# Performance work log

Measured on AMD Instinct MI355X. Metric: run time of the kernel, lower is better.

Reference implementation:

```python
import jax, jax.numpy as jnp
import numpy as np

B, N, D, E, H = 4, 512, 16, 16, 128  # envs, max_node, node_dim, edge_dim, hidden_dim


def setup_inputs() -> dict:
    key = jax.random.key(0)
    ks = jax.random.split(key, 8)
    node_feature = jax.random.normal(ks[0], (B, N, D), dtype=jnp.float32)
    adjacency = (jax.random.uniform(ks[1], (B, N, N)) < 0.05).astype(jnp.float32)
    edge_feature = jax.random.normal(ks[2], (B, N, N, E), dtype=jnp.float32)
    node_mask = jnp.ones((B, N), dtype=jnp.float32)  # unused by the model, kept for signature parity
    # edge_fc: Dense(2*D + E -> H) with relu; feature_fc: Dense(H + D -> H) with relu
    W_edge = jax.random.normal(ks[3], (2 * D + E, H), dtype=jnp.float32) * np.sqrt(2.0 / (2 * D + E)).astype(np.float32)
    b_edge = jnp.zeros((H,), dtype=jnp.float32)
    W_feat = jax.random.normal(ks[4], (H + D, H), dtype=jnp.float32) * np.sqrt(2.0 / (H + D)).astype(np.float32)
    b_feat = jnp.zeros((H,), dtype=jnp.float32)
    return {
        "node_feature": node_feature,
        "adjacency": adjacency,
        "edge_feature": edge_feature,
        "node_mask": node_mask,
        "W_edge": W_edge,
        "b_edge": b_edge,
        "W_feat": W_feat,
        "b_feat": b_feat,
    }


def reference(node_feature, adjacency, edge_feature, node_mask, W_edge, b_edge, W_feat, b_feat):
    d = node_feature.shape[-1]
    # Split edge_fc weight by the concat layout [node_i, node_j, edge]:
    # concat([node_i, node_j, edge]) @ W == node_i@Wi + node_j@Wj + edge@We
    Wi, Wj, We = W_edge[:d], W_edge[d:2 * d], W_edge[2 * d:]
    proj_i = jnp.einsum("bnd,dh->bnh", node_feature, Wi)  # sender (row) projection
    proj_j = jnp.einsum("bnd,dh->bnh", node_feature, Wj)  # receiver (col) projection
    proj_e = jnp.einsum("bije,eh->bijh", edge_feature, We)
    edge_out = jax.nn.relu(proj_i[:, :, None, :] + proj_j[:, None, :, :] + proj_e + b_edge)  # (B,N,N,H)
    # adjacency-masked sum over neighbors j (axis=2)
    message = jnp.einsum("bijh,bij->bih", edge_out, adjacency)  # (B,N,H)
    ending = jax.nn.relu(jnp.concatenate([message, node_feature], axis=-1) @ W_feat + b_feat)  # (B,N,H)
    return ending, edge_out
```

## Files before the change

kernel.cpp:

```cpp
#include <hip/hip_runtime.h>

#define BB 4
#define NN 512
#define DD 16
#define EE 16
#define HH 128

typedef float f32x4 __attribute__((ext_vector_type(4)));

#define LD4(p) (*(const float4*)(p))

__global__ void proj_j_kernel(const float* __restrict__ nf,
                              const float* __restrict__ W_edge,
                              float* __restrict__ pj) {
    int idx = blockIdx.x * 256 + threadIdx.x;
    if (idx >= BB * NN * HH) return;
    int h  = idx & (HH - 1);
    int bj = idx >> 7;
    const float* row = nf + bj * DD;
    float acc = 0.f;
#pragma unroll
    for (int d = 0; d < DD; ++d)
        acc = fmaf(row[d], W_edge[(DD + d) * HH + h], acc);
    pj[idx] = acc;
}

template <bool USE_WS>
__global__ __launch_bounds__(128, 4)
void fused_kernel(const float* __restrict__ node_feature,
                  const float* __restrict__ adjacency,
                  const float* __restrict__ edge_feature,
                  const float* __restrict__ W_edge,
                  const float* __restrict__ b_edge,
                  const float* __restrict__ W_feat,
                  const float* __restrict__ b_feat,
                  const float* __restrict__ pj,
                  float* __restrict__ out_end,
                  float* __restrict__ out_edge) {
    const int bi = blockIdx.x;
    const int b  = bi >> 9;
    const int t  = threadIdx.x;
    const int hq = t & 31;
    const int jl = t >> 5;
    const int h0 = hq * 4;

    float4 we[EE];
#pragma unroll
    for (int e = 0; e < EE; ++e)
        we[e] = LD4(W_edge + (2 * DD + e) * HH + h0);

    float4 wj[USE_WS ? 1 : EE];
    if constexpr (!USE_WS) {
#pragma unroll
        for (int e = 0; e < EE; ++e)
            wj[e] = LD4(W_edge + (DD + e) * HH + h0);
    }

    float4 pi = LD4(b_edge + h0);
    {
        const float* nfi = node_feature + bi * DD;
#pragma unroll
        for (int d4 = 0; d4 < DD; d4 += 4) {
            float4 v = LD4(nfi + d4);
            float nd[4] = {v.x, v.y, v.z, v.w};
#pragma unroll
            for (int q = 0; q < 4; ++q) {
                float4 wi = LD4(W_edge + (d4 + q) * HH + h0);
                pi.x = fmaf(nd[q], wi.x, pi.x);
                pi.y = fmaf(nd[q], wi.y, pi.y);
                pi.z = fmaf(nd[q], wi.z, pi.z);
                pi.w = fmaf(nd[q], wi.w, pi.w);
            }
        }
    }

    const float* efb  = edge_feature + (size_t)bi * NN * EE;
    const float* adjr = adjacency + (size_t)bi * NN;
    const float* pjb  = pj + (b * NN) * HH;
    const float* nfb  = node_feature + (b * NN) * DD;
    float*       eob  = out_edge + (size_t)bi * NN * HH;

    float4 msg = make_float4(0.f, 0.f, 0.f, 0.f);

    int j = jl;
    float4 efA0 = LD4(efb + j * EE + 0);
    float4 efA1 = LD4(efb + j * EE + 4);
    float4 efA2 = LD4(efb + j * EE + 8);
    float4 efA3 = LD4(efb + j * EE + 12);
    float4 pjA  = make_float4(0.f, 0.f, 0.f, 0.f);
    if constexpr (USE_WS) pjA = LD4(pjb + j * HH + h0);
    float  adjA = adjr[j];

    for (int it = 0; it < NN / 4; ++it) {
        const int jn = j + 4;
        const int jc = (jn < NN) ? jn : j;

        float4 efB0 = LD4(efb + jc * EE + 0);
        float4 efB1 = LD4(efb + jc * EE + 4);
        float4 efB2 = LD4(efb + jc * EE + 8);
        float4 efB3 = LD4(efb + jc * EE + 12);
        float4 pjB  = make_float4(0.f, 0.f, 0.f, 0.f);
        if constexpr (USE_WS) pjB = LD4(pjb + jc * HH + h0);
        float  adjB = adjr[jc];

        float4 acc;
        if constexpr (USE_WS) {
            acc.x = pi.x + pjA.x;
            acc.y = pi.y + pjA.y;
            acc.z = pi.z + pjA.z;
            acc.w = pi.w + pjA.w;
        } else {
            acc = pi;
            const float* nfj = nfb + j * DD;
#pragma unroll
            for (int d = 0; d < DD; ++d) {
                float nv = nfj[d];
                acc.x = fmaf(nv, wj[d].x, acc.x);
                acc.y = fmaf(nv, wj[d].y, acc.y);
                acc.z = fmaf(nv, wj[d].z, acc.z);
                acc.w = fmaf(nv, wj[d].w, acc.w);
            }
        }

        float ef_[EE] = {efA0.x, efA0.y, efA0.z, efA0.w,
                         efA1.x, efA1.y, efA1.z, efA1.w,
                         efA2.x, efA2.y, efA2.z, efA2.w,
                         efA3.x, efA3.y, efA3.z, efA3.w};
#pragma unroll
        for (int e = 0; e < EE; ++e) {
            acc.x = fmaf(ef_[e], we[e].x, acc.x);
            acc.y = fmaf(ef_[e], we[e].y, acc.y);
            acc.z = fmaf(ef_[e], we[e].z, acc.z);
            acc.w = fmaf(ef_[e], we[e].w, acc.w);
        }
        acc.x = fmaxf(acc.x, 0.f);
        acc.y = fmaxf(acc.y, 0.f);
        acc.z = fmaxf(acc.z, 0.f);
        acc.w = fmaxf(acc.w, 0.f);

        __builtin_nontemporal_store((f32x4){acc.x, acc.y, acc.z, acc.w},
                                    (f32x4*)(eob + (size_t)j * HH + h0));

        msg.x = fmaf(adjA, acc.x, msg.x);
        msg.y = fmaf(adjA, acc.y, msg.y);
        msg.z = fmaf(adjA, acc.z, msg.z);
        msg.w = fmaf(adjA, acc.w, msg.w);

        efA0 = efB0; efA1 = efB1; efA2 = efB2; efA3 = efB3;
        pjA = pjB; adjA = adjB;
        j = jn;
    }

    __shared__ float msgred[4][HH];
    *(float4*)&msgred[jl][h0] = msg;
    __syncthreads();

    if (jl == 0) {
        float4 acc = LD4(b_feat + h0);
#pragma unroll 4
        for (int k = 0; k < HH; ++k) {
            float m = msgred[0][k] + msgred[1][k] + msgred[2][k] + msgred[3][k];
            float4 w = LD4(W_feat + k * HH + h0);
            acc.x = fmaf(m, w.x, acc.x);
            acc.y = fmaf(m, w.y, acc.y);
            acc.z = fmaf(m, w.z, acc.z);
            acc.w = fmaf(m, w.w, acc.w);
        }
        const float* nfi = node_feature + bi * DD;
#pragma unroll
        for (int d = 0; d < DD; ++d) {
            float m = nfi[d];
            float4 w = LD4(W_feat + (HH + d) * HH + h0);
            acc.x = fmaf(m, w.x, acc.x);
            acc.y = fmaf(m, w.y, acc.y);
            acc.z = fmaf(m, w.z, acc.z);
            acc.w = fmaf(m, w.w, acc.w);
        }
        acc.x = fmaxf(acc.x, 0.f);
        acc.y = fmaxf(acc.y, 0.f);
        acc.z = fmaxf(acc.z, 0.f);
        acc.w = fmaxf(acc.w, 0.f);
        *(float4*)(out_end + bi * HH + h0) = acc;
    }
}

extern "C" void kernel_launch(void* const* d_in, const int* in_sizes, int n_in,
                              void* d_out, int out_size, void* d_ws, size_t ws_size,
                              hipStream_t stream) {
    const float* node_feature = (const float*)d_in[0];
    const float* adjacency    = (const float*)d_in[1];
    const float* edge_feature = (const float*)d_in[2];
    const float* W_edge = (const float*)d_in[4];
    const float* b_edge = (const float*)d_in[5];
    const float* W_feat = (const float*)d_in[6];
    const float* b_feat = (const float*)d_in[7];

    float* out_end  = (float*)d_out;
    float* out_edge = out_end + (size_t)BB * NN * HH;

    const size_t pj_bytes = (size_t)BB * NN * HH * sizeof(float);
    if (ws_size >= pj_bytes) {
        float* pj = (float*)d_ws;
        proj_j_kernel<<<(BB * NN * HH + 255) / 256, 256, 0, stream>>>(
            node_feature, W_edge, pj);
        fused_kernel<true><<<BB * NN, 128, 0, stream>>>(
            node_feature, adjacency, edge_feature, W_edge, b_edge,
            W_feat, b_feat, pj, out_end, out_edge);
    } else {
        fused_kernel<false><<<BB * NN, 128, 0, stream>>>(
            node_feature, adjacency, edge_feature, W_edge, b_edge,
            W_feat, b_feat, nullptr, out_end, out_edge);
    }
}
```

Baseline: 140.3 us.

## Batch four neighbor rows per iteration to raise memory-level parallelism

The inner loop now loads edge features, pj rows and adjacency for four neighbors at once, computes all four outputs, then issues four nontemporal stores together. This replaces the previous one-ahead software prefetch. The goal is more loads in flight per wave to hide global latency. Launch bounds drop from 4 to 2 blocks per SIMD so the extra live registers fit, which may lower occupancy. The fallback path now reloads wj from memory instead of keeping it in registers.

```diff
diff --git a/kernel.cpp b/kernel.cpp
--- a/kernel.cpp
+++ b/kernel.cpp
@@ -26,7 +26,7 @@
 }
 
 template <bool USE_WS>
-__global__ __launch_bounds__(128, 4)
+__global__ __launch_bounds__(128, 2)
 void fused_kernel(const float* __restrict__ node_feature,
                   const float* __restrict__ adjacency,
                   const float* __restrict__ edge_feature,
@@ -49,13 +49,6 @@
     for (int e = 0; e < EE; ++e)
         we[e] = LD4(W_edge + (2 * DD + e) * HH + h0);
 
-    float4 wj[USE_WS ? 1 : EE];
-    if constexpr (!USE_WS) {
-#pragma unroll
-        for (int e = 0; e < EE; ++e)
-            wj[e] = LD4(W_edge + (DD + e) * HH + h0);
-    }
-
     float4 pi = LD4(b_edge + h0);
     {
         const float* nfi = node_feature + bi * DD;
@@ -82,73 +75,73 @@
 
     float4 msg = make_float4(0.f, 0.f, 0.f, 0.f);
 
-    int j = jl;
-    float4 efA0 = LD4(efb + j * EE + 0);
-    float4 efA1 = LD4(efb + j * EE + 4);
-    float4 efA2 = LD4(efb + j * EE + 8);
-    float4 efA3 = LD4(efb + j * EE + 12);
-    float4 pjA  = make_float4(0.f, 0.f, 0.f, 0.f);
-    if constexpr (USE_WS) pjA = LD4(pjb + j * HH + h0);
-    float  adjA = adjr[j];
-
-    for (int it = 0; it < NN / 4; ++it) {
-        const int jn = j + 4;
-        const int jc = (jn < NN) ? jn : j;
-
-        float4 efB0 = LD4(efb + jc * EE + 0);
-        float4 efB1 = LD4(efb + jc * EE + 4);
-        float4 efB2 = LD4(efb + jc * EE + 8);
-        float4 efB3 = LD4(efb + jc * EE + 12);
-        float4 pjB  = make_float4(0.f, 0.f, 0.f, 0.f);
-        if constexpr (USE_WS) pjB = LD4(pjb + jc * HH + h0);
-        float  adjB = adjr[jc];
-
-        float4 acc;
-        if constexpr (USE_WS) {
-            acc.x = pi.x + pjA.x;
-            acc.y = pi.y + pjA.y;
-            acc.z = pi.z + pjA.z;
-            acc.w = pi.w + pjA.w;
-        } else {
-            acc = pi;
-            const float* nfj = nfb + j * DD;
-#pragma unroll
-            for (int d = 0; d < DD; ++d) {
-                float nv = nfj[d];
-                acc.x = fmaf(nv, wj[d].x, acc.x);
-                acc.y = fmaf(nv, wj[d].y, acc.y);
-                acc.z = fmaf(nv, wj[d].z, acc.z);
-                acc.w = fmaf(nv, wj[d].w, acc.w);
+    for (int it = 0; it < NN / 16; ++it) {
+        const int jb = 16 * it + jl;
+
+        float4 ef[4][4];
+        float4 pjv[4];
+        float  adjv[4];
+#pragma unroll
+        for (int r = 0; r < 4; ++r) {
+            const int j = jb + 4 * r;
+#pragma unroll
+            for (int q = 0; q < 4; ++q)
+                ef[r][q] = LD4(efb + j * EE + 4 * q);
+            if constexpr (USE_WS) pjv[r] = LD4(pjb + j * HH + h0);
+            adjv[r] = adjr[j];
+        }
+
+        float4 accr[4];
+#pragma unroll
+        for (int r = 0; r < 4; ++r) {
+            float4 acc;
+            if constexpr (USE_WS) {
+                acc.x = pi.x + pjv[r].x;
+                acc.y = pi.y + pjv[r].y;
+                acc.z = pi.z + pjv[r].z;
+                acc.w = pi.w + pjv[r].w;
+            } else {
+                acc = pi;
+                const float* nfj = nfb + (jb + 4 * r) * DD;
+#pragma unroll
+                for (int d = 0; d < DD; ++d) {
+                    float nv = nfj[d];
+                    float4 wj = LD4(W_edge + (DD + d) * HH + h0);
+                    acc.x = fmaf(nv, wj.x, acc.x);
+                    acc.y = fmaf(nv, wj.y, acc.y);
+                    acc.z = fmaf(nv, wj.z, acc.z);
+                    acc.w = fmaf(nv, wj.w, acc.w);
+                }
             }
-        }
-
-        float ef_[EE] = {efA0.x, efA0.y, efA0.z, efA0.w,
-                         efA1.x, efA1.y, efA1.z, efA1.w,
-                         efA2.x, efA2.y, efA2.z, efA2.w,
-                         efA3.x, efA3.y, efA3.z, efA3.w};
-#pragma unroll
-        for (int e = 0; e < EE; ++e) {
-            acc.x = fmaf(ef_[e], we[e].x, acc.x);
-            acc.y = fmaf(ef_[e], we[e].y, acc.y);
-            acc.z = fmaf(ef_[e], we[e].z, acc.z);
-            acc.w = fmaf(ef_[e], we[e].w, acc.w);
-        }
-        acc.x = fmaxf(acc.x, 0.f);
-        acc.y = fmaxf(acc.y, 0.f);
-        acc.z = fmaxf(acc.z, 0.f);
-        acc.w = fmaxf(acc.w, 0.f);
-
-        __builtin_nontemporal_store((f32x4){acc.x, acc.y, acc.z, acc.w},
-                                    (f32x4*)(eob + (size_t)j * HH + h0));
-
-        msg.x = fmaf(adjA, acc.x, msg.x);
-        msg.y = fmaf(adjA, acc.y, msg.y);
-        msg.z = fmaf(adjA, acc.z, msg.z);
-        msg.w = fmaf(adjA, acc.w, msg.w);
-
-        efA0 = efB0; efA1 = efB1; efA2 = efB2; efA3 = efB3;
-        pjA = pjB; adjA = adjB;
-        j = jn;
+#pragma unroll
+            for (int q = 0; q < 4; ++q) {
+                float ev[4] = {ef[r][q].x, ef[r][q].y, ef[r][q].z, ef[r][q].w};
+#pragma unroll
+                for (int u = 0; u < 4; ++u) {
+                    acc.x = fmaf(ev[u], we[4 * q + u].x, acc.x);
+                    acc.y = fmaf(ev[u], we[4 * q + u].y, acc.y);
+                    acc.z = fmaf(ev[u], we[4 * q + u].z, acc.z);
+                    acc.w = fmaf(ev[u], we[4 * q + u].w, acc.w);
+                }
+            }
+            acc.x = fmaxf(acc.x, 0.f);
+            acc.y = fmaxf(acc.y, 0.f);
+            acc.z = fmaxf(acc.z, 0.f);
+            acc.w = fmaxf(acc.w, 0.f);
+            accr[r] = acc;
+
+            msg.x = fmaf(adjv[r], acc.x, msg.x);
+            msg.y = fmaf(adjv[r], acc.y, msg.y);
+            msg.z = fmaf(adjv[r], acc.z, msg.z);
+            msg.w = fmaf(adjv[r], acc.w, msg.w);
+        }
+
+#pragma unroll
+        for (int r = 0; r < 4; ++r) {
+            __builtin_nontemporal_store(
+                (f32x4){accr[r].x, accr[r].y, accr[r].z, accr[r].w},
+                (f32x4*)(eob + (size_t)(jb + 4 * r) * HH + h0));
+        }
     }
 
     __shared__ float msgred[4][HH];
```

Measured after the change: 138.7 us. No clear change (-1.2%).
